# Optimization experiments

Measured on AMD Instinct MI355X. Metric: run time of the kernel, lower is better.

The kernel has to match this reference:

```python
import jax, jax.numpy as jnp
import numpy as np

B, D, H, S = 32768, 512, 8, 3  # batch, stream_dim, heads, num_streams
DH = D // H
EPS = 1e-5


def setup_inputs() -> dict:
    key = jax.random.key(0)
    ks = jax.random.split(key, 16)
    sc = lambda fan_in: 1.0 / np.sqrt(fan_in)
    return {
        "kinematic_h": jax.random.normal(ks[0], (B, D), jnp.float32),
        "color_h": jax.random.normal(ks[1], (B, D), jnp.float32),
        "spinor_h": jax.random.normal(ks[2], (B, D), jnp.float32),
        # MultiheadAttention packed in-proj and out-proj
        "w_in": jax.random.normal(ks[3], (3 * D, D), jnp.float32) * sc(D),
        "b_in": jnp.zeros((3 * D,), jnp.float32),
        "w_out": jax.random.normal(ks[4], (D, D), jnp.float32) * sc(D),
        "b_out": jnp.zeros((D,), jnp.float32),
        # stream gate: Linear(3D -> 3) + softmax
        "w_gate": jax.random.normal(ks[5], (S, S * D), jnp.float32) * sc(S * D),
        "b_gate": jnp.zeros((S,), jnp.float32),
        # fusion MLP: Linear(3D -> 2D), SiLU, Linear(2D -> D)
        "w1": jax.random.normal(ks[6], (2 * D, S * D), jnp.float32) * sc(S * D),
        "b1": jnp.zeros((2 * D,), jnp.float32),
        "w2": jax.random.normal(ks[7], (D, 2 * D), jnp.float32) * sc(2 * D),
        "b2": jnp.zeros((D,), jnp.float32),
        # LayerNorm
        "gamma": jnp.ones((D,), jnp.float32),
        "beta": jnp.zeros((D,), jnp.float32),
    }


def reference(kinematic_h, color_h, spinor_h, w_in, b_in, w_out, b_out,
              w_gate, b_gate, w1, b1, w2, b2, gamma, beta):
    stacked = jnp.stack([kinematic_h, color_h, spinor_h], axis=1)  # [B,S,D]
    b = stacked.shape[0]
    # self-attention (Q=K=V=stacked), packed QKV projection
    qkv = stacked @ w_in.T + b_in  # [B,S,3D]
    q, k, v = jnp.split(qkv, 3, axis=-1)
    q = q.reshape(b, S, H, DH)
    k = k.reshape(b, S, H, DH)
    v = v.reshape(b, S, H, DH)
    scores = jnp.einsum("bqhd,bkhd->bhqk", q, k) / np.sqrt(DH)
    attn = jax.nn.softmax(scores, axis=-1)
    out = jnp.einsum("bhqk,bkhd->bqhd", attn, v).reshape(b, S, D)
    attn_out = stacked + (out @ w_out.T + b_out)  # residual, [B,S,D]
    # gating softmax over streams
    flat = attn_out.reshape(b, S * D)
    gates = jax.nn.softmax(flat @ w_gate.T + b_gate, axis=-1)[..., None]  # [B,S,1]
    gated = (attn_out * gates).reshape(b, S * D)
    # fusion MLP (dropout=eval no-op)
    h = jax.nn.silu(gated @ w1.T + b1)
    fused = h @ w2.T + b2  # [B,D]
    # LayerNorm
    mu = jnp.mean(fused, axis=-1, keepdims=True)
    var = jnp.var(fused, axis=-1, keepdims=True)
    return (fused - mu) * jax.lax.rsqrt(var + EPS) * gamma + beta
```

## Files before the change

kernel.cpp:

```cpp
#include <hip/hip_runtime.h>
#include <hip/hip_bf16.h>
#include <stdint.h>


typedef float f32x4 __attribute__((ext_vector_type(4)));
typedef short bf16x8 __attribute__((ext_vector_type(8)));

__device__ __forceinline__ float bf2f(unsigned short h) {
  return __uint_as_float(((unsigned)h) << 16);
}
__device__ __forceinline__ unsigned short f2bf(float f) {
  __hip_bfloat16 h = __float2bfloat16(f);
  return *reinterpret_cast<unsigned short*>(&h);
}
__device__ __forceinline__ unsigned pack2bf(float lo, float hi) {
  __hip_bfloat162 h2 = __float22bfloat162_rn(make_float2(lo, hi));
  return *reinterpret_cast<unsigned*>(&h2);
}
__device__ __forceinline__ uint2 f2bf4p(float4 v) {
  return make_uint2(pack2bf(v.x, v.y), pack2bf(v.z, v.w));
}

__device__ __forceinline__ void async_cp16(const void* g, void* lds) {
  __builtin_amdgcn_global_load_lds(
      (const __attribute__((address_space(1))) void*)g,
      (__attribute__((address_space(3))) void*)lds, 16, 0, 0);
}

__global__ void __launch_bounds__(256) cvtall(const float4* __restrict__ w_in,
                                              const float4* __restrict__ w_out,
                                              const float4* __restrict__ w1,
                                              const float4* __restrict__ w2,
                                              uint2* __restrict__ dst) {
  int i = blockIdx.x * 256 + threadIdx.x;
  const float4* s;
  int off;
  if (i < 196608)      { s = w_in;  off = 0; }
  else if (i < 262144) { s = w_out; off = 196608; }
  else if (i < 655360) { s = w1;    off = 262144; }
  else                 { s = w2;    off = 655360; }
  dst[i] = f2bf4p(s[i - off]);
}

__global__ void __launch_bounds__(256)
qkv_attn(const float* __restrict__ X0,
         const float* __restrict__ X1,
         const float* __restrict__ X2,
         const unsigned short* __restrict__ Wi,
         const float* __restrict__ bin,
         unsigned short* __restrict__ Sout,
         unsigned short* __restrict__ AO) {
  __shared__ unsigned short lds[96 * 200];
  unsigned short* Abuf = lds;
  unsigned short* Bbuf = lds + 6144;

  const int t = threadIdx.x;
  const int lane = t & 63;
  const int wave = t >> 6;
  const int wm = wave >> 1, wn = wave & 1;

  const int ny = gridDim.y;
  const int id = blockIdx.y * 8 + blockIdx.x;
  const int xcd = id & 7, j = id >> 3;
  const int h = j & 7;
  const long m0 = (long)(xcd * (ny >> 3) + (j >> 3)) * 96;

  const int trow = t >> 3;
  const int swz = ((t & 7) ^ (trow & 7)) << 3;
  const long b0 = m0 / 3;
  const float* Aptr[3];
  unsigned short* Sptr[3];
#pragma unroll
  for (int r = 0; r < 3; r++) {
    const int rl = trow + 32 * r;
    const int br = rl / 3;
    const int sr = rl - 3 * br;
    const float* X = (sr == 0) ? X0 : (sr == 1) ? X1 : X2;
    Aptr[r] = X + (b0 + br) * 512 + swz;
    Sptr[r] = Sout + (m0 + rl) * 512 + swz;
  }
  const unsigned short* Bg = Wi + ((long)h * 64 + trow) * 512 + swz;
  unsigned short* AsD = Abuf + t * 8;
  unsigned short* BsD = Bbuf + t * 8;

  f32x4 acc[3][6] = {};
  const int arow0 = wm * 48 + (lane & 15);
  const int brow0 = wn * 96 + (lane & 15);

  float4 Alo[3], Ahi[3];
#pragma unroll
  for (int r = 0; r < 3; r++) {
    Alo[r] = *(const float4*)(Aptr[r]);
    Ahi[r] = *(const float4*)(Aptr[r] + 4);
  }

  for (int k0 = 0; k0 < 512; k0 += 64) {
    __syncthreads();
    const bool sw = ((k0 >> 6) == h);
#pragma unroll
    for (int r = 0; r < 3; r++) {
      const uint4 uv = make_uint4(
          pack2bf(Alo[r].x, Alo[r].y), pack2bf(Alo[r].z, Alo[r].w),
          pack2bf(Ahi[r].x, Ahi[r].y), pack2bf(Ahi[r].z, Ahi[r].w));
      *(uint4*)(AsD + r * 2048) = uv;
      if (sw) *(uint4*)(Sptr[r] + k0) = uv;
    }
#pragma unroll
    for (int r = 0; r < 6; r++)
      async_cp16(Bg + (long)((r >> 1) * 512 + (r & 1) * 32) * 512 + k0, BsD + r * 2048);
    __syncthreads();
    if (k0 + 64 < 512) {
#pragma unroll
      for (int r = 0; r < 3; r++) {
        Alo[r] = *(const float4*)(Aptr[r] + k0 + 64);
        Ahi[r] = *(const float4*)(Aptr[r] + k0 + 68);
      }
    }
#pragma unroll
    for (int kk = 0; kk < 2; kk++) {
      const int sc = ((kk * 4 + (lane >> 4)) ^ (lane & 7)) << 3;
      bf16x8 af[3], bfr[6];
#pragma unroll
      for (int mt = 0; mt < 3; mt++)
        af[mt] = *(const bf16x8*)&Abuf[(arow0 + mt * 16) * 64 + sc];
#pragma unroll
      for (int nt = 0; nt < 6; nt++)
        bfr[nt] = *(const bf16x8*)&Bbuf[(brow0 + nt * 16) * 64 + sc];
#pragma unroll
      for (int mt = 0; mt < 3; mt++)
#pragma unroll
        for (int nt = 0; nt < 6; nt++)
          acc[mt][nt] = __builtin_amdgcn_mfma_f32_16x16x32_bf16(
              af[mt], bfr[nt], acc[mt][nt], 0, 0, 0);
    }
  }

  __syncthreads();
  const int crow0 = wm * 48 + ((lane >> 4) << 2);
  const int ccol0 = wn * 96 + (lane & 15);
#pragma unroll
  for (int nt = 0; nt < 6; nt++) {
    const int col = ccol0 + nt * 16;
    const float bv = bin[(col >> 6) * 512 + h * 64 + (col & 63)];
#pragma unroll
    for (int mt = 0; mt < 3; mt++) {
      const int rb = (crow0 + mt * 16) * 200 + col;
      const unsigned p01 = pack2bf(acc[mt][nt][0] + bv, acc[mt][nt][1] + bv);
      const unsigned p23 = pack2bf(acc[mt][nt][2] + bv, acc[mt][nt][3] + bv);
      lds[rb]       = (unsigned short)p01;
      lds[rb + 200] = (unsigned short)(p01 >> 16);
      lds[rb + 400] = (unsigned short)p23;
      lds[rb + 600] = (unsigned short)(p23 >> 16);
    }
  }
  __syncthreads();

  const int bi = lane >> 3;
  const int l8 = lane & 7;
  const int r0 = (wave * 8 + bi) * 3;
  float q[3][8], k[3][8], v[3][8];
#pragma unroll
  for (int s = 0; s < 3; s++) {
    const unsigned short* rowp = &lds[(r0 + s) * 200 + l8 * 8];
    uint4 qu = *(const uint4*)(rowp);
    uint4 ku = *(const uint4*)(rowp + 64);
    uint4 vu = *(const uint4*)(rowp + 128);
    const unsigned* qw = (const unsigned*)&qu;
    const unsigned* kw = (const unsigned*)&ku;
    const unsigned* vw = (const unsigned*)&vu;
#pragma unroll
    for (int jj = 0; jj < 4; jj++) {
      q[s][2 * jj]     = __uint_as_float(qw[jj] << 16);
      q[s][2 * jj + 1] = __uint_as_float(qw[jj] & 0xffff0000u);
      k[s][2 * jj]     = __uint_as_float(kw[jj] << 16);
      k[s][2 * jj + 1] = __uint_as_float(kw[jj] & 0xffff0000u);
      v[s][2 * jj]     = __uint_as_float(vw[jj] << 16);
      v[s][2 * jj + 1] = __uint_as_float(vw[jj] & 0xffff0000u);
    }
  }
  float p[3][3];
#pragma unroll
  for (int s = 0; s < 3; s++)
#pragma unroll
    for (int u = 0; u < 3; u++) {
      float d = 0.f;
#pragma unroll
      for (int e = 0; e < 8; e++) d = fmaf(q[s][e], k[u][e], d);
      p[s][u] = d;
    }
#pragma unroll
  for (int m = 1; m < 8; m <<= 1)
#pragma unroll
    for (int s = 0; s < 3; s++)
#pragma unroll
      for (int u = 0; u < 3; u++) p[s][u] += __shfl_xor(p[s][u], m, 64);

  unsigned short* ob = AO + (m0 + r0) * 512 + h * 64 + l8 * 8;
#pragma unroll
  for (int s = 0; s < 3; s++) {
    float a0 = p[s][0] * 0.125f, a1 = p[s][1] * 0.125f, a2 = p[s][2] * 0.125f;
    float mx = fmaxf(a0, fmaxf(a1, a2));
    float e0 = __expf(a0 - mx), e1 = __expf(a1 - mx), e2 = __expf(a2 - mx);
    float inv = 1.0f / (e0 + e1 + e2);
    unsigned ow[4];
#pragma unroll
    for (int jj = 0; jj < 4; jj++) {
      float lo = (e0 * v[0][2 * jj] + e1 * v[1][2 * jj] + e2 * v[2][2 * jj]) * inv;
      float hi = (e0 * v[0][2 * jj + 1] + e1 * v[1][2 * jj + 1] + e2 * v[2][2 * jj + 1]) * inv;
      ow[jj] = pack2bf(lo, hi);
    }
    *(uint4*)(ob + s * 512) = *(uint4*)ow;
  }
}

enum { EPI_BF16 = 0, EPI_RES = 1, EPI_SILU = 2, EPI_F32 = 3 };

template <int EPI>
__global__ void __launch_bounds__(256)
gemm_bt(const unsigned short* __restrict__ A,
        const unsigned short* __restrict__ W,
        const float* __restrict__ bias,
        const unsigned short* __restrict__ Res,
        void* __restrict__ Out,
        int K, int N) {
  __shared__ unsigned short As[128 * 64];
  __shared__ unsigned short Bs[128 * 64];
  const int t = threadIdx.x;
  const int lane = t & 63;
  const int wave = t >> 6;
  const int wm = wave >> 1, wn = wave & 1;

  const int nb = gridDim.x;
  const int nblocks = nb * gridDim.y;
  const int id = blockIdx.y * nb + blockIdx.x;
  const int lid = ((nblocks & 7) == 0) ? ((id & 7) * (nblocks >> 3) + (id >> 3)) : id;
  const long bm = (long)(lid / nb) * 128;
  const long bn = (long)(lid % nb) * 128;

  const int srow = t >> 3;
  const int schunk = ((t & 7) ^ (srow & 7)) << 3;
  const unsigned short* Ag = A + (bm + srow) * (long)K + schunk;
  const unsigned short* Wg = W + (bn + srow) * (long)K + schunk;
  unsigned short* AsD = As + t * 8;
  unsigned short* BsD = Bs + t * 8;

  f32x4 acc[4][4] = {};
  const int arow0 = wm * 64 + (lane & 15);
  const int brow0 = wn * 64 + (lane & 15);

  for (int k0 = 0; k0 < K; k0 += 64) {
    __syncthreads();
#pragma unroll
    for (int i = 0; i < 4; i++) {
      async_cp16(Ag + (long)(i * 32) * K + k0, AsD + i * 2048);
      async_cp16(Wg + (long)(i * 32) * K + k0, BsD + i * 2048);
    }
    __syncthreads();
#pragma unroll
    for (int kk = 0; kk < 2; kk++) {
      const int sc = ((kk * 4 + (lane >> 4)) ^ (lane & 7)) << 3;
      bf16x8 af[4], bfr[4];
#pragma unroll
      for (int mt = 0; mt < 4; mt++)
        af[mt] = *(const bf16x8*)&As[(arow0 + mt * 16) * 64 + sc];
#pragma unroll
      for (int nt = 0; nt < 4; nt++)
        bfr[nt] = *(const bf16x8*)&Bs[(brow0 + nt * 16) * 64 + sc];
#pragma unroll
      for (int mt = 0; mt < 4; mt++)
#pragma unroll
        for (int nt = 0; nt < 4; nt++)
          acc[mt][nt] = __builtin_amdgcn_mfma_f32_16x16x32_bf16(
              af[mt], bfr[nt], acc[mt][nt], 0, 0, 0);
    }
  }

  const long row0 = bm + wm * 64 + ((lane >> 4) << 2);
  const int col0 = (int)bn + wn * 64 + (lane & 15);
#pragma unroll
  for (int nt = 0; nt < 4; nt++) {
    const int col = col0 + nt * 16;
    const float bv = bias[col];
#pragma unroll
    for (int mt = 0; mt < 4; mt++) {
      const long rbase = row0 + mt * 16;
#pragma unroll
      for (int r = 0; r < 4; r++) {
        float v = acc[mt][nt][r] + bv;
        const long idx = (rbase + r) * (long)N + col;
        if (EPI == EPI_RES) v += bf2f(Res[idx]);
        if (EPI == EPI_SILU) v = v * (1.0f / (1.0f + __expf(-v)));
        if (EPI == EPI_F32)
          ((float*)Out)[idx] = v;
        else
          ((unsigned short*)Out)[idx] = f2bf(v);
      }
    }
  }
}

__global__ void __launch_bounds__(256) gate3(const unsigned short* AT,
                                             const float* __restrict__ WG,
                                             const float* __restrict__ BG,
                                             unsigned short* G) {
  int row = blockIdx.x * 4 + (threadIdx.x >> 6);
  int lane = threadIdx.x & 63;
  const unsigned short* rp = AT + (long)row * 1536 + lane * 8;
  float x[3][8];
  float p[3] = {0.f, 0.f, 0.f};
#pragma unroll
  for (int seg = 0; seg < 3; seg++) {
    uint4 u = *(const uint4*)(rp + seg * 512);
    const unsigned* uw = (const unsigned*)&u;
#pragma unroll
    for (int j = 0; j < 4; j++) {
      x[seg][2 * j]     = __uint_as_float(uw[j] << 16);
      x[seg][2 * j + 1] = __uint_as_float(uw[j] & 0xffff0000u);
    }
    const int e0 = seg * 512 + lane * 8;
#pragma unroll
    for (int g = 0; g < 3; g++) {
      const float* wp = WG + g * 1536 + e0;
#pragma unroll
      for (int e = 0; e < 8; e++) p[g] = fmaf(x[seg][e], wp[e], p[g]);
    }
  }
#pragma unroll
  for (int m = 1; m < 64; m <<= 1)
#pragma unroll
    for (int g = 0; g < 3; g++) p[g] += __shfl_xor(p[g], m, 64);
  float g0 = p[0] + BG[0], g1 = p[1] + BG[1], g2 = p[2] + BG[2];
  float mx = fmaxf(g0, fmaxf(g1, g2));
  g0 = __expf(g0 - mx); g1 = __expf(g1 - mx); g2 = __expf(g2 - mx);
  float inv = 1.0f / (g0 + g1 + g2);
  float gs[3] = {g0 * inv, g1 * inv, g2 * inv};
  unsigned short* op = G + (long)row * 1536 + lane * 8;
#pragma unroll
  for (int seg = 0; seg < 3; seg++) {
    unsigned ow[4];
#pragma unroll
    for (int j = 0; j < 4; j++)
      ow[j] = pack2bf(x[seg][2 * j] * gs[seg], x[seg][2 * j + 1] * gs[seg]);
    *(uint4*)(op + seg * 512) = *(uint4*)ow;
  }
}

__global__ void __launch_bounds__(256) lnorm(const float* __restrict__ F,
                                             const float* __restrict__ gamma,
                                             const float* __restrict__ beta,
                                             float* __restrict__ out) {
  int row = blockIdx.x * 4 + (threadIdx.x >> 6);
  int lane = threadIdx.x & 63;
  const float4* fr = (const float4*)(F + (long)row * 512);
  float4 a = fr[lane], c = fr[lane + 64];
  float s = a.x + a.y + a.z + a.w + c.x + c.y + c.z + c.w;
  float ss = a.x * a.x + a.y * a.y + a.z * a.z + a.w * a.w +
             c.x * c.x + c.y * c.y + c.z * c.z + c.w * c.w;
#pragma unroll
  for (int m = 1; m < 64; m <<= 1) {
    s += __shfl_xor(s, m, 64);
    ss += __shfl_xor(ss, m, 64);
  }
  float mean = s * (1.0f / 512.0f);
  float var = ss * (1.0f / 512.0f) - mean * mean;
  float rstd = rsqrtf(var + 1e-5f);
  const float4* g4 = (const float4*)gamma;
  const float4* b4 = (const float4*)beta;
  float4 g0 = g4[lane], g1 = g4[lane + 64], be0 = b4[lane], be1 = b4[lane + 64];
  float4 o0, o1;
  o0.x = (a.x - mean) * rstd * g0.x + be0.x;
  o0.y = (a.y - mean) * rstd * g0.y + be0.y;
  o0.z = (a.z - mean) * rstd * g0.z + be0.z;
  o0.w = (a.w - mean) * rstd * g0.w + be0.w;
  o1.x = (c.x - mean) * rstd * g1.x + be1.x;
  o1.y = (c.y - mean) * rstd * g1.y + be1.y;
  o1.z = (c.z - mean) * rstd * g1.z + be1.z;
  o1.w = (c.w - mean) * rstd * g1.w + be1.w;
  float4* orow = (float4*)(out + (long)row * 512);
  orow[lane] = o0;
  orow[lane + 64] = o1;
}

extern "C" void kernel_launch(void* const* d_in, const int* in_sizes, int n_in,
                              void* d_out, int out_size, void* d_ws, size_t ws_size,
                              hipStream_t stream) {
  const float* kin    = (const float*)d_in[0];
  const float* colr   = (const float*)d_in[1];
  const float* spi    = (const float*)d_in[2];
  const float* w_in   = (const float*)d_in[3];
  const float* b_in   = (const float*)d_in[4];
  const float* w_out  = (const float*)d_in[5];
  const float* b_out  = (const float*)d_in[6];
  const float* w_gate = (const float*)d_in[7];
  const float* b_gate = (const float*)d_in[8];
  const float* w1     = (const float*)d_in[9];
  const float* b1     = (const float*)d_in[10];
  const float* w2     = (const float*)d_in[11];
  const float* b2     = (const float*)d_in[12];
  const float* gamma  = (const float*)d_in[13];
  const float* beta   = (const float*)d_in[14];
  float* out = (float*)d_out;

  long Bc = 32768;
  while (Bc > 1024 && (size_t)(6291456 + 9216 * Bc) > ws_size) Bc >>= 1;
  const int nch = (int)(32768 / Bc);

  char* ws = (char*)d_ws;
  unsigned short* Wic = (unsigned short*)(ws);
  unsigned short* Woc = (unsigned short*)(ws + 1572864);
  unsigned short* W1c = (unsigned short*)(ws + 2097152);
  unsigned short* W2c = (unsigned short*)(ws + 5242880);
  char* Sb  = ws + 6291456;
  char* AOb = Sb + 3072 * Bc;
  char* ATb = AOb + 3072 * Bc;

  cvtall<<<3072, 256, 0, stream>>>((const float4*)w_in, (const float4*)w_out,
                                   (const float4*)w1, (const float4*)w2,
                                   (uint2*)ws);

  for (int c = 0; c < nch; c++) {
    const long boff = (long)c * Bc;
    unsigned short* S_c  = (unsigned short*)Sb;
    unsigned short* AO_c = (unsigned short*)AOb;
    unsigned short* AT_c = (unsigned short*)ATb;
    unsigned short* G_c  = AT_c;
    unsigned short* H_c  = (unsigned short*)AOb;
    float*          F_c  = (float*)Sb;

    qkv_attn<<<dim3(8, (int)(Bc / 32)), 256, 0, stream>>>(
        kin + boff * 512, colr + boff * 512, spi + boff * 512,
        Wic, b_in, S_c, AO_c);
    gemm_bt<EPI_RES><<<dim3(4, (int)(3 * Bc / 128)), 256, 0, stream>>>(
        AO_c, Woc, b_out, S_c, AT_c, 512, 512);
    gate3<<<(int)(Bc / 4), 256, 0, stream>>>(AT_c, w_gate, b_gate, G_c);
    gemm_bt<EPI_SILU><<<dim3(8, (int)(Bc / 128)), 256, 0, stream>>>(
        G_c, W1c, b1, nullptr, H_c, 1536, 1024);
    gemm_bt<EPI_F32><<<dim3(4, (int)(Bc / 128)), 256, 0, stream>>>(
        H_c, W2c, b2, nullptr, F_c, 1024, 512);
    lnorm<<<(int)(Bc / 4), 256, 0, stream>>>(F_c, gamma, beta, out + boff * 512);
  }
}
```

Before: 774.4 us.

## Fuse final MLP GEMM with LayerNorm into one full-row kernel

Replaces the second MLP GEMM (fp32 output) plus the separate LayerNorm kernel with a single kernel in which each 512-thread block computes 64 full output rows of 512 columns. Row statistics are reduced across waves through shared memory, and the normalized result is written straight to the output. This removes the fp32 intermediate write and reread and one launch per chunk. In exchange the block tile is smaller in M and unpipelined, with a large B tile in LDS (64 KB+) that may limit occupancy. The output stores are strided scalar writes.

```diff
diff --git a/kernel.cpp b/kernel.cpp
--- a/kernel.cpp
+++ b/kernel.cpp
@@ -299,6 +299,116 @@
   }
 }
 
+__global__ void __launch_bounds__(512)
+gemm_ln(const unsigned short* __restrict__ A,
+        const unsigned short* __restrict__ W,
+        const float* __restrict__ bias,
+        const float* __restrict__ gamma,
+        const float* __restrict__ beta,
+        float* __restrict__ Out,
+        int K) {
+  __shared__ unsigned short As[64 * 64];
+  __shared__ unsigned short Bs[512 * 64];
+  __shared__ float stats[8][64][2];
+  const int t = threadIdx.x;
+  const int lane = t & 63;
+  const int wave = t >> 6;
+
+  const int nblocks = gridDim.x;
+  const int id = blockIdx.x;
+  const int lid = ((nblocks & 7) == 0) ? ((id & 7) * (nblocks >> 3) + (id >> 3)) : id;
+  const long bm = (long)lid * 64;
+
+  const int srow = t >> 3;
+  const int sch = ((t & 7) ^ (srow & 7)) << 3;
+  const unsigned short* Ag = A + (bm + srow) * (long)K + sch;
+  const unsigned short* Wg = W + (long)srow * K + sch;
+  unsigned short* AsD = As + t * 8;
+  unsigned short* BsD = Bs + t * 8;
+
+  f32x4 acc[4][4] = {};
+  const int arow0 = lane & 15;
+  const int brow0 = wave * 64 + (lane & 15);
+
+  for (int k0 = 0; k0 < K; k0 += 64) {
+    __syncthreads();
+    async_cp16(Ag + k0, AsD);
+#pragma unroll
+    for (int i = 0; i < 8; i++)
+      async_cp16(Wg + (long)(i * 64) * K + k0, BsD + i * 4096);
+    __syncthreads();
+#pragma unroll
+    for (int kk = 0; kk < 2; kk++) {
+      const int sc = ((kk * 4 + (lane >> 4)) ^ (lane & 7)) << 3;
+      bf16x8 af[4], bfr[4];
+#pragma unroll
+      for (int mt = 0; mt < 4; mt++)
+        af[mt] = *(const bf16x8*)&As[(arow0 + mt * 16) * 64 + sc];
+#pragma unroll
+      for (int nt = 0; nt < 4; nt++)
+        bfr[nt] = *(const bf16x8*)&Bs[(brow0 + nt * 16) * 64 + sc];
+#pragma unroll
+      for (int mt = 0; mt < 4; mt++)
+#pragma unroll
+        for (int nt = 0; nt < 4; nt++)
+          acc[mt][nt] = __builtin_amdgcn_mfma_f32_16x16x32_bf16(
+              af[mt], bfr[nt], acc[mt][nt], 0, 0, 0);
+    }
+  }
+
+  const int colb = wave * 64 + (lane & 15);
+  float bv[4], gm[4], be[4];
+#pragma unroll
+  for (int nt = 0; nt < 4; nt++) {
+    bv[nt] = bias[colb + nt * 16];
+    gm[nt] = gamma[colb + nt * 16];
+    be[nt] = beta[colb + nt * 16];
+  }
+#pragma unroll
+  for (int mt = 0; mt < 4; mt++)
+#pragma unroll
+    for (int r = 0; r < 4; r++) {
+      float s = 0.f, ss = 0.f;
+#pragma unroll
+      for (int nt = 0; nt < 4; nt++) {
+        const float v = acc[mt][nt][r] + bv[nt];
+        s += v; ss += v * v;
+      }
+#pragma unroll
+      for (int m = 1; m < 16; m <<= 1) {
+        s += __shfl_xor(s, m, 64);
+        ss += __shfl_xor(ss, m, 64);
+      }
+      if ((lane & 15) == 0) {
+        const int rl = mt * 16 + ((lane >> 4) << 2) + r;
+        stats[wave][rl][0] = s;
+        stats[wave][rl][1] = ss;
+      }
+    }
+  __syncthreads();
+#pragma unroll
+  for (int mt = 0; mt < 4; mt++)
+#pragma unroll
+    for (int r = 0; r < 4; r++) {
+      const int rl = mt * 16 + ((lane >> 4) << 2) + r;
+      float s = 0.f, ss = 0.f;
+#pragma unroll
+      for (int w = 0; w < 8; w++) {
+        s += stats[w][rl][0];
+        ss += stats[w][rl][1];
+      }
+      const float mean = s * (1.0f / 512.0f);
+      const float var = ss * (1.0f / 512.0f) - mean * mean;
+      const float rstd = rsqrtf(var + 1e-5f);
+      float* orow = Out + (bm + rl) * 512;
+#pragma unroll
+      for (int nt = 0; nt < 4; nt++) {
+        const float v = acc[mt][nt][r] + bv[nt];
+        orow[colb + nt * 16] = (v - mean) * rstd * gm[nt] + be[nt];
+      }
+    }
+}
+
 __global__ void __launch_bounds__(256) gate3(const unsigned short* AT,
                                              const float* __restrict__ WG,
                                              const float* __restrict__ BG,
@@ -343,42 +453,6 @@
       ow[j] = pack2bf(x[seg][2 * j] * gs[seg], x[seg][2 * j + 1] * gs[seg]);
     *(uint4*)(op + seg * 512) = *(uint4*)ow;
   }
-}
-
-__global__ void __launch_bounds__(256) lnorm(const float* __restrict__ F,
-                                             const float* __restrict__ gamma,
-                                             const float* __restrict__ beta,
-                                             float* __restrict__ out) {
-  int row = blockIdx.x * 4 + (threadIdx.x >> 6);
-  int lane = threadIdx.x & 63;
-  const float4* fr = (const float4*)(F + (long)row * 512);
-  float4 a = fr[lane], c = fr[lane + 64];
-  float s = a.x + a.y + a.z + a.w + c.x + c.y + c.z + c.w;
-  float ss = a.x * a.x + a.y * a.y + a.z * a.z + a.w * a.w +
-             c.x * c.x + c.y * c.y + c.z * c.z + c.w * c.w;
-#pragma unroll
-  for (int m = 1; m < 64; m <<= 1) {
-    s += __shfl_xor(s, m, 64);
-    ss += __shfl_xor(ss, m, 64);
-  }
-  float mean = s * (1.0f / 512.0f);
-  float var = ss * (1.0f / 512.0f) - mean * mean;
-  float rstd = rsqrtf(var + 1e-5f);
-  const float4* g4 = (const float4*)gamma;
-  const float4* b4 = (const float4*)beta;
-  float4 g0 = g4[lane], g1 = g4[lane + 64], be0 = b4[lane], be1 = b4[lane + 64];
-  float4 o0, o1;
-  o0.x = (a.x - mean) * rstd * g0.x + be0.x;
-  o0.y = (a.y - mean) * rstd * g0.y + be0.y;
-  o0.z = (a.z - mean) * rstd * g0.z + be0.z;
-  o0.w = (a.w - mean) * rstd * g0.w + be0.w;
-  o1.x = (c.x - mean) * rstd * g1.x + be1.x;
-  o1.y = (c.y - mean) * rstd * g1.y + be1.y;
-  o1.z = (c.z - mean) * rstd * g1.z + be1.z;
-  o1.w = (c.w - mean) * rstd * g1.w + be1.w;
-  float4* orow = (float4*)(out + (long)row * 512);
-  orow[lane] = o0;
-  orow[lane + 64] = o1;
 }
 
 extern "C" void kernel_launch(void* const* d_in, const int* in_sizes, int n_in,
@@ -425,7 +499,6 @@
     unsigned short* AT_c = (unsigned short*)ATb;
     unsigned short* G_c  = AT_c;
     unsigned short* H_c  = (unsigned short*)AOb;
-    float*          F_c  = (float*)Sb;
 
     qkv_attn<<<dim3(8, (int)(Bc / 32)), 256, 0, stream>>>(
         kin + boff * 512, colr + boff * 512, spi + boff * 512,
@@ -435,8 +508,7 @@
     gate3<<<(int)(Bc / 4), 256, 0, stream>>>(AT_c, w_gate, b_gate, G_c);
     gemm_bt<EPI_SILU><<<dim3(8, (int)(Bc / 128)), 256, 0, stream>>>(
         G_c, W1c, b1, nullptr, H_c, 1536, 1024);
-    gemm_bt<EPI_F32><<<dim3(4, (int)(Bc / 128)), 256, 0, stream>>>(
-        H_c, W2c, b2, nullptr, F_c, 1024, 512);
-    lnorm<<<(int)(Bc / 4), 256, 0, stream>>>(F_c, gamma, beta, out + boff * 512);
-  }
-}
+    gemm_ln<<<(int)(Bc / 64), 512, 0, stream>>>(
+        H_c, W2c, b2, gamma, beta, out + boff * 512, 1024);
+  }
+}
```

After: 782.8 us. No clear change (+1.1%).
